# Performance work log

Measured on AMD Instinct MI355X. Metric: run time of the kernel, lower is better.

The kernel has to match this reference:

```python
import jax, jax.numpy as jnp
import numpy as np
import math

B, T, C = 2, 1024, 1024
H = 16
HS = C // H          # head size 64
ROT = HS // 2        # rotary dims 32
TT = 1024            # ctx_len
FFN = 4 * C
EPS = 1e-6


def _layernorm(x, g, b):
    m = jnp.mean(x, -1, keepdims=True)
    v = jnp.mean((x - m) ** 2, -1, keepdims=True)
    return (x - m) * jax.lax.rsqrt(v + EPS) * g + b


def _time_shift_half(x):
    # ZeroPad2d((0,0,1,-1)) applied to first half of channels: shift by one step in time
    c = x.shape[-1]
    a = jnp.pad(x[:, :, : c // 2], ((0, 0), (1, 0), (0, 0)))[:, :-1, :]
    return jnp.concatenate([a, x[:, :, c // 2 :]], axis=-1)


def _rotate_half(x):
    x1, x2 = jnp.split(x, 2, axis=-1)
    return jnp.concatenate([-x2, x1], axis=-1)


def _rotary_cos_sin(t_len, rot, base):
    inv_freq = 1.0 / (base ** (jnp.arange(0, rot, 2, dtype=jnp.float32) / rot))
    freqs = jnp.arange(t_len, dtype=jnp.float32)[:, None] * inv_freq[None, :]
    emb = jnp.concatenate([freqs, freqs], axis=-1)  # (T, rot)
    return jnp.cos(emb), jnp.sin(emb)


def _build_w(time_w, time_alpha, time_beta, t_len):
    # faithful translation of the pad/tile/reshape circulant trick
    w = jnp.pad(time_w, ((0, 0), (0, TT)))            # (H, 2TT)
    w = jnp.tile(w, (1, TT))                          # (H, 2TT*TT)
    w = w[:, :-TT].reshape(-1, TT, 2 * TT - 1)        # (H, TT, 2TT-1)
    w = w[:, :, TT - 1 :]                             # (H, TT, TT)
    return w[:, :t_len, :t_len] * time_alpha[:, :, :t_len] * time_beta[:, :t_len, :]


def setup_inputs() -> dict:
    key = jax.random.key(0)
    ks = jax.random.split(key, 24)
    s = 0.02
    d = {
        "x": jax.random.normal(ks[0], (B, T, C), jnp.float32),
        "ln1_g": jnp.ones((C,), jnp.float32),
        "ln1_b": jnp.zeros((C,), jnp.float32),
        "Wq": jax.random.normal(ks[1], (C, C), jnp.float32) * s,
        "bq": jnp.zeros((C,), jnp.float32),
        "Wk": jax.random.normal(ks[2], (C, C), jnp.float32) * s,
        "bk": jnp.zeros((C,), jnp.float32),
        "Wv": jax.random.normal(ks[3], (C, C), jnp.float32) * s,
        "bv": jnp.zeros((C,), jnp.float32),
        "Wo": jax.random.normal(ks[4], (C, C), jnp.float32) * s,
        "bo": jnp.zeros((C,), jnp.float32),
        "time_w": 1.0 + 0.01 * jax.random.normal(ks[5], (H, TT), jnp.float32),
        "time_alpha": 1.0 + 0.01 * jax.random.normal(ks[6], (H, 1, TT), jnp.float32),
        "time_beta": 1.0 + 0.01 * jax.random.normal(ks[7], (H, TT, 1), jnp.float32),
        "time_gamma": 1.0 + 0.01 * jax.random.normal(ks[8], (TT, 1), jnp.float32),
        "Wmix": jnp.eye(H, dtype=jnp.float32) + 0.01 * jax.random.normal(ks[9], (H, H), jnp.float32),
        "ln2_g": jnp.ones((C,), jnp.float32),
        "ln2_b": jnp.zeros((C,), jnp.float32),
        "Wgk": jax.random.normal(ks[10], (C, FFN), jnp.float32) * s,
        "bgk": jnp.zeros((FFN,), jnp.float32),
        "Wgv": jax.random.normal(ks[11], (C, FFN), jnp.float32) * s,
        "bgv": jnp.zeros((FFN,), jnp.float32),
        "Wgw": jax.random.normal(ks[12], (FFN, C), jnp.float32) * s,
        "bgw": jnp.zeros((C,), jnp.float32),
    }
    return d


def _block(x, ln1_g, ln1_b, Wq, bq, Wk, bk, Wv, bv, Wo, bo,
           time_w, time_alpha, time_beta, time_gamma, Wmix,
           ln2_g, ln2_b, Wgk, bgk, Wgv, bgv, Wgw, bgw):
    b, t, c = x.shape
    # ---- MHA_pro attention sublayer (pre-LN residual) ----
    xs = _time_shift_half(_layernorm(x, ln1_g, ln1_b))
    q = (xs @ Wq + bq).reshape(b, t, H, HS).transpose(0, 2, 1, 3)  # bhtd
    k = (xs @ Wk + bk).reshape(b, t, H, HS).transpose(0, 2, 1, 3)
    v = (xs @ Wv + bv).reshape(b, t, H, HS).transpose(0, 2, 1, 3)
    qr, qp = q[..., :ROT], q[..., ROT:]
    kr, kp = k[..., :ROT], k[..., ROT:]
    cos, sin = _rotary_cos_sin(t, ROT, float(TT))  # base = ctx_len
    qr = qr * cos + _rotate_half(qr) * sin
    kr = kr * cos + _rotate_half(kr) * sin
    q = jnp.concatenate([qr, qp], axis=-1)
    k = jnp.concatenate([kr, kp], axis=-1)
    att = jnp.einsum("bhtd,bhud->bhtu", q, k) * (1.0 / math.sqrt(HS))
    causal = jnp.tril(jnp.ones((t, t), bool))
    att = jnp.where(causal, att, -jnp.inf)
    att = jax.nn.softmax(att, axis=-1)
    w = _build_w(time_w, time_alpha, time_beta, t)  # (H, T, T)
    att = att * w[None]
    att = jnp.einsum("ij,bjtu->bitu", Wmix, att)  # 1x1 conv head mix
    y = jnp.einsum("bhtu,bhud->bhtd", att, v)
    y = y.transpose(0, 2, 1, 3).reshape(b, t, c)
    y = (y @ Wo + bo) * time_gamma[:t, :]
    x = x + y
    # ---- GeGLU MLP sublayer (pre-LN residual) ----
    xm = _layernorm(x, ln2_g, ln2_b)
    kk = xm @ Wgk + bgk
    vv = xm @ Wgv + bgv
    y2 = (jax.nn.gelu(kk, approximate=False) * vv) @ Wgw + bgw
    return x + y2


def reference(x, ln1_g, ln1_b, Wq, bq, Wk, bk, Wv, bv, Wo, bo,
              time_w, time_alpha, time_beta, time_gamma, Wmix,
              ln2_g, ln2_b, Wgk, bgk, Wgv, bgv, Wgw, bgw):
    return _block(x, ln1_g, ln1_b, Wq, bq, Wk, bk, Wv, bv, Wo, bo,
                  time_w, time_alpha, time_beta, time_gamma, Wmix,
                  ln2_g, ln2_b, Wgk, bgk, Wgv, bgv, Wgw, bgw)
```

## Files before the change

kernel.cpp:

```cpp
#include <hip/hip_runtime.h>
#include <math.h>

typedef unsigned short u16;
typedef short s16x8 __attribute__((ext_vector_type(8)));
typedef float f32x4 __attribute__((ext_vector_type(4)));

#define TB 2
#define TSEQ 1024
#define CC 1024
#define NH 16
#define HSZ 64
#define FFN 4096
#define MROWS (TB*TSEQ)

#define GLOAD16(g, l) __builtin_amdgcn_global_load_lds( \
    (const __attribute__((address_space(1))) unsigned*)(g), \
    (__attribute__((address_space(3))) unsigned*)(l), 16, 0, 0)

#define SBAR()  __builtin_amdgcn_s_barrier()
#define SCHED0() __builtin_amdgcn_sched_barrier(0)
#define LGKM0() asm volatile("s_waitcnt lgkmcnt(0)" ::: "memory")
#define WAITV4() asm volatile("s_waitcnt vmcnt(4)" ::: "memory")
#define PRIO(n) __builtin_amdgcn_s_setprio(n)

__device__ __forceinline__ float bf2f(u16 u){
  union { unsigned u; float f; } c; c.u = ((unsigned)u) << 16; return c.f;
}
__device__ __forceinline__ u16 f2bf(float f){
  union { float f; unsigned u; } c; c.f = f;
  unsigned u = c.u;
  u += 0x7fffu + ((u >> 16) & 1);
  return (u16)(u >> 16);
}
__device__ __forceinline__ float ldin(const void* p, size_t i, int bf){
  return bf ? bf2f(((const u16*)p)[i]) : ((const float*)p)[i];
}

__global__ void k_flag(const unsigned* __restrict__ g, int* __restrict__ flag){
  if (threadIdx.x == 0) *flag = (g[0] == 0x3F800000u) ? 0 : 1;
}

struct Prep {
  const void* csrc[10]; u16* cdst[10]; int cp0[11];
  const void* tw; u16* tw8; float2* rt;
};
__global__ void k_prep(Prep P, const int* __restrict__ flagp){
  int bf = *flagp;
  int blk = blockIdx.x, tid = threadIdx.x;
  if (blk < 184){
    int idx = blk*256 + tid;
    int s = 0;
    #pragma unroll
    for (int i = 1; i < 10; i++) if (idx >= P.cp0[i]) s = i;
    int r = idx - P.cp0[s];
    P.cdst[s][r] = f2bf(ldin(P.csrc[s], r, bf));
  } else if (blk < 696){
    int idx = (blk-184)*256 + tid;
    int s = idx >> 14;
    int h = (idx >> 10) & 15;
    int k = idx & 1023;
    float v = (k + s < 1024) ? ldin(P.tw, h*1024 + k + s, bf) : 0.f;
    P.tw8[idx] = f2bf(v);
  } else {
    int idx = (blk-696)*256 + tid;
    int i = idx & 15, t = idx >> 4;
    float invf = exp2f(-0.625f * (float)i);
    float ang = (float)t * invf;
    P.rt[idx] = (float2){cosf(ang), sinf(ang)};
  }
}

struct TEnt { const void* src; u16* dst; int R, C, bxn, blk0; };
struct TPack { TEnt e[7]; };
__global__ void k_transpose_all(TPack p, const int* __restrict__ flagp){
  int bf = *flagp;
  __shared__ u16 tile[32][33];
  int blk = blockIdx.x;
  int ei = 0;
  #pragma unroll
  for (int i = 1; i < 7; i++) if (blk >= p.e[i].blk0) ei = i;
  const void* src = p.e[ei].src;
  u16* dst = p.e[ei].dst;
  int R = p.e[ei].R, C = p.e[ei].C;
  int rel = blk - p.e[ei].blk0;
  int bx = (rel % p.e[ei].bxn) * 32, by = (rel / p.e[ei].bxn) * 32;
  int tx = threadIdx.x & 31, ty = threadIdx.x >> 5;
  #pragma unroll
  for (int i = 0; i < 32; i += 8)
    tile[ty + i][tx] = f2bf(ldin(src, (size_t)(by + ty + i) * C + bx + tx, bf));
  __syncthreads();
  #pragma unroll
  for (int i = 0; i < 32; i += 8)
    dst[(size_t)(bx + ty + i) * R + by + tx] = tile[tx][ty + i];
}

__global__ void k_ln1_shift(const void* __restrict__ x, const void* __restrict__ g,
                            const void* __restrict__ bta, u16* __restrict__ xs,
                            const int* __restrict__ flagp){
  int bf = *flagp;
  int row = blockIdx.x;
  int t = row & (TSEQ - 1);
  int tid = threadIdx.x;
  int wv = tid >> 6, lane = tid & 63;
  float v[4]; float s = 0.f, ss = 0.f;
  #pragma unroll
  for (int i = 0; i < 4; i++){
    v[i] = ldin(x, (size_t)row * CC + tid*4 + i, bf);
    s += v[i]; ss += v[i]*v[i];
  }
  #pragma unroll
  for (int o = 32; o > 0; o >>= 1){ s += __shfl_xor(s, o); ss += __shfl_xor(ss, o); }
  __shared__ float rs[4], rss[4];
  if (lane == 0){ rs[wv] = s; rss[wv] = ss; }
  __syncthreads();
  float S = rs[0]+rs[1]+rs[2]+rs[3];
  float SS = rss[0]+rss[1]+rss[2]+rss[3];
  float mean = S * (1.0f/CC);
  float var  = SS * (1.0f/CC) - mean*mean;
  float inv  = rsqrtf(var + 1e-6f);
  #pragma unroll
  for (int i = 0; i < 4; i++){
    int c = tid*4 + i;
    float o = (v[i]-mean)*inv*ldin(g, c, bf) + ldin(bta, c, bf);
    u16 ob = f2bf(o);
    if (c >= CC/2)            xs[(size_t)row*CC + c] = ob;
    else if (t < TSEQ-1)      xs[(size_t)(row+1)*CC + c] = ob;
  }
  if (t == 0 && tid < 128){
    #pragma unroll
    for (int i = 0; i < 4; i++) xs[(size_t)row*CC + tid*4 + i] = 0;
  }
}

__global__ __launch_bounds__(256) void k_qk(
    const u16* __restrict__ qkv, u16* __restrict__ att)
{
  int m0 = blockIdx.y * 128;
  int n0 = blockIdx.x * 128;
  if (n0 > m0) return;
  int bh = blockIdx.z; int b = bh >> 4, h = bh & 15;
  __shared__ u16 As[128*32];
  __shared__ u16 Bs[128*32];
  int tid = threadIdx.x;
  int w = tid >> 6;
  int lane = tid & 63;
  int wm = (w >> 1) * 64, wn = (w & 1) * 64;
  f32x4 acc[4][4];
  #pragma unroll
  for (int i = 0; i < 4; i++)
    #pragma unroll
    for (int j = 0; j < 4; j++) acc[i][j] = (f32x4){0.f,0.f,0.f,0.f};

  int rr = lane >> 2;
  int cc = lane & 3;
  const u16* gA0 = qkv + (size_t)(b*TSEQ + m0 + w*32 + rr)*(3*CC) + h*HSZ + cc*8;
  const u16* gA1 = gA0 + (size_t)16*(3*CC);
  const u16* gB0 = qkv + (size_t)(b*TSEQ + n0 + w*32 + rr)*(3*CC) + CC + h*HSZ + cc*8;
  const u16* gB1 = gB0 + (size_t)16*(3*CC);
  u16* lA0 = As + (w*32)*32;
  u16* lA1 = As + (w*32+16)*32;
  u16* lB0 = Bs + (w*32)*32;
  u16* lB1 = Bs + (w*32+16)*32;
  int quad = lane >> 4;
  int l15 = lane & 15;

  #pragma unroll
  for (int k0 = 0; k0 < HSZ; k0 += 32){
    __syncthreads();
    GLOAD16(gA0 + k0, lA0);
    GLOAD16(gA1 + k0, lA1);
    GLOAD16(gB0 + k0, lB0);
    GLOAD16(gB1 + k0, lB1);
    __syncthreads();
    s16x8 af[4], bfr[4];
    #pragma unroll
    for (int i = 0; i < 4; i++){
      af[i]  = *(s16x8*)&As[(wm + i*16 + l15)*32 + quad*8];
      bfr[i] = *(s16x8*)&Bs[(wn + i*16 + l15)*32 + quad*8];
    }
    #pragma unroll
    for (int mi = 0; mi < 4; mi++)
      #pragma unroll
      for (int ni = 0; ni < 4; ni++)
        acc[mi][ni] = __builtin_amdgcn_mfma_f32_16x16x32_bf16(af[mi], bfr[ni], acc[mi][ni], 0, 0, 0);
  }

  #pragma unroll
  for (int mi = 0; mi < 4; mi++){
    int rowb = m0 + wm + mi*16 + quad*4;
    #pragma unroll
    for (int ni = 0; ni < 4; ni++){
      int col = n0 + wn + ni*16 + l15;
      #pragma unroll
      for (int r = 0; r < 4; r++){
        int t = rowb + r;
        att[((size_t)bh*TSEQ + t)*TSEQ + col] = f2bf(acc[mi][ni][r] * 0.125f);
      }
    }
  }
}

__global__ __launch_bounds__(1024) void k_softmix(
    u16* __restrict__ att, const u16* __restrict__ tw8, const u16* __restrict__ al16,
    const u16* __restrict__ be16, const void* __restrict__ wmix,
    const int* __restrict__ flagp)
{
  int bf = *flagp;
  int bt = blockIdx.x;
  int t = bt & (TSEQ-1);
  int b = bt >> 10;
  int tid = threadIdx.x;
  int h = tid >> 6;
  int lane = tid & 63;
  int tile_end = ((t >> 7) + 1) << 7;
  int nchunk = (t >> 9) + 1;
  int sh = (TSEQ-1 - t) & 7;
  int base = (TSEQ-1 - t) - sh;
  __shared__ __align__(16) u16 P[NH][TSEQ];
  __shared__ float wm[NH*NH];
  if (tid < NH*NH) wm[tid] = ldin(wmix, tid, bf);

  {
    const u16* srow = att + ((size_t)(b*NH + h)*TSEQ + t)*TSEQ;
    const u16* twp  = tw8 + ((size_t)sh*NH + h)*TSEQ + base;
    const u16* alp  = al16 + h*TSEQ;
    float v[16];
    float lmax = -1e30f;
    for (int r = 0; r < nchunk; r++){
      int ub = lane*8 + r*512;
      uint4 pk = *(const uint4*)(srow + ub);
      const u16* pe = (const u16*)&pk;
      #pragma unroll
      for (int e = 0; e < 8; e++){
        float s = bf2f(pe[e]);
        if (ub + e > t) s = -1e30f;
        v[r*8+e] = s;
        lmax = fmaxf(lmax, s);
      }
    }
    #pragma unroll
    for (int o = 32; o > 0; o >>= 1) lmax = fmaxf(lmax, __shfl_xor(lmax, o));
    float lsum = 0.f;
    for (int r = 0; r < nchunk; r++){
      #pragma unroll
      for (int e = 0; e < 8; e++){
        float p = __expf(v[r*8+e] - lmax);
        v[r*8+e] = p; lsum += p;
      }
    }
    #pragma unroll
    for (int o = 32; o > 0; o >>= 1) lsum += __shfl_xor(lsum, o);
    float btv = bf2f(be16[h*TSEQ + t]);
    float inv = btv / lsum;
    for (int r = 0; r < nchunk; r++){
      int ub = lane*8 + r*512;
      uint4 wk = *(const uint4*)(twp + ub);
      uint4 ak = *(const uint4*)(alp + ub);
      const u16* we = (const u16*)&wk;
      const u16* ae = (const u16*)&ak;
      u16 tmp[8];
      #pragma unroll
      for (int e = 0; e < 8; e++){
        float p = v[r*8+e] * inv * bf2f(we[e]) * bf2f(ae[e]);
        tmp[e] = f2bf(p);
      }
      *(uint4*)&P[h][ub] = *(uint4*)tmp;
    }
  }
  __syncthreads();

  int u0 = tid * 2;
  if (u0 < tile_end){
    float a0_[16], a1_[16];
    #pragma unroll
    for (int i = 0; i < 16; i++){ a0_[i] = 0.f; a1_[i] = 0.f; }
    #pragma unroll
    for (int j = 0; j < 16; j++){
      unsigned pk = *(const unsigned*)&P[j][u0];
      float p0 = bf2f((u16)(pk & 0xffff)), p1 = bf2f((u16)(pk >> 16));
      #pragma unroll
      for (int i = 0; i < 16; i++){
        float w = wm[i*NH + j];
        a0_[i] += w*p0; a1_[i] += w*p1;
      }
    }
    #pragma unroll
    for (int i = 0; i < 16; i++){
      u16 tmp[2] = {f2bf(a0_[i]), f2bf(a1_[i])};
      *(unsigned*)(att + ((size_t)(b*NH + i)*TSEQ + t)*TSEQ + u0) = *(unsigned*)tmp;
    }
  }
}

__global__ void k_vt(const u16* __restrict__ qkv, u16* __restrict__ vt){
  __shared__ u16 tile[32][33];
  int bh = blockIdx.z; int b = bh >> 4, h = bh & 15;
  int u0 = blockIdx.x * 32, d0 = blockIdx.y * 32;
  int tx = threadIdx.x & 31, ty = threadIdx.x >> 5;
  #pragma unroll
  for (int i = 0; i < 32; i += 8)
    tile[ty + i][tx] = qkv[(size_t)(b*TSEQ + u0 + ty + i)*(3*CC) + 2*CC + h*HSZ + d0 + tx];
  __syncthreads();
  #pragma unroll
  for (int i = 0; i < 32; i += 8)
    vt[((size_t)bh*HSZ + d0 + ty + i)*TSEQ + u0 + tx] = tile[tx][ty + i];
}

__global__ void k_gelumul(const u16* __restrict__ kkvv, u16* __restrict__ hh){
  int idx = blockIdx.x*256 + threadIdx.x;
  int m = idx >> 9;
  int j = (idx & 511) * 8;
  uint4 kk4 = *(const uint4*)(kkvv + (size_t)m*(2*FFN) + j);
  uint4 vv4 = *(const uint4*)(kkvv + (size_t)m*(2*FFN) + FFN + j);
  const u16* ks = (const u16*)&kk4;
  const u16* vs = (const u16*)&vv4;
  u16 out[8];
  #pragma unroll
  for (int e = 0; e < 8; e++){
    float kk = bf2f(ks[e]), vv = bf2f(vs[e]);
    float ge = 0.5f*kk*(1.0f + erff(kk*0.70710678f));
    out[e] = f2bf(ge*vv);
  }
  *(uint4*)(hh + (size_t)m*FFN + j) = *(uint4*)out;
}

__global__ __launch_bounds__(512, 2) void k_gemm256(
    const u16* __restrict__ A, const u16* __restrict__ Bt,
    const u16* __restrict__ bias, int M, int N, int K, int mode,
    u16* __restrict__ outp, float* __restrict__ partial,
    const float2* __restrict__ rt)
{
  __shared__ u16 S[65536];
  u16* SA0 = S;
  u16* SB0 = S + 16384;
  u16* SA1 = S + 32768;
  u16* SB1 = S + 49152;

  int nwg = (int)(gridDim.x * gridDim.y * gridDim.z);
  int lin = (int)(blockIdx.x + gridDim.x * (blockIdx.y + gridDim.y * blockIdx.z));
  int nl  = (nwg & 7) ? lin : ((lin & 7) * (nwg >> 3) + (lin >> 3));
  int bx  = nl % (int)gridDim.x;
  int tq  = nl / (int)gridDim.x;
  int by  = tq % (int)gridDim.y;
  int bz  = tq / (int)gridDim.y;

  int m0 = by * 256, n0 = bx * 256;
  int kper = K / (int)gridDim.z;
  int kbeg = bz * kper;
  int nt = kper >> 6;
  int niter = nt >> 1;

  int tid = threadIdx.x;
  int w = tid >> 6, lane = tid & 63;
  int wm = w >> 2, wn = w & 3;
  int quad = lane >> 4, l15 = lane & 15;
  int l3 = lane >> 3, ch = (lane & 7) ^ l3;

  const u16* gA = A  + (size_t)(m0 + w*16 + l3) * K + ch*8 + kbeg;
  const u16* gB = Bt + (size_t)(n0 + w*16 + l3) * K + ch*8 + kbeg;
  const size_t hstep = (size_t)128 * K;
  const size_t rstep = (size_t)8 * K;

  int pc0 = quad ^ (l15 & 7);
  int pc1 = (4 + quad) ^ (l15 & 7);
  int aoff0 = (wm*128 + l15)*64 + pc0*8;
  int aoff1 = (wm*128 + l15)*64 + pc1*8;
  int boff0 = (wn*64 + l15)*64 + pc0*8;
  int boff1 = (wn*64 + l15)*64 + pc1*8;

  f32x4 acc[8][4];
  #pragma unroll
  for (int i = 0; i < 8; i++)
    #pragma unroll
    for (int j = 0; j < 4; j++) acc[i][j] = (f32x4){0.f,0.f,0.f,0.f};

  #define STG(gbase, sbase, h, ko) do{ \
      const u16* _g = (gbase) + (size_t)(h)*hstep + (ko); \
      u16* _l = (sbase) + ((h)*128 + w*16)*64; \
      GLOAD16(_g, _l); \
      GLOAD16(_g + rstep, _l + 512); \
    }while(0)

  #define LD_A(buf, MQ) do{ _Pragma("unroll") for (int _m = 0; _m < 4; _m++){ \
      a0[_m] = *(const s16x8*)((buf) + aoff0 + (MQ)*4096 + _m*1024); \
      a1[_m] = *(const s16x8*)((buf) + aoff1 + (MQ)*4096 + _m*1024); } }while(0)

  #define LD_B(buf, NQ, B0A, B1A) do{ _Pragma("unroll") for (int _n = 0; _n < 2; _n++){ \
      B0A[_n] = *(const s16x8*)((buf) + boff0 + (NQ)*2048 + _n*1024); \
      B1A[_n] = *(const s16x8*)((buf) + boff1 + (NQ)*2048 + _n*1024); } }while(0)

  #define MMQ(MQ, NQ, B0A, B1A) do{ _Pragma("unroll") for (int _m = 0; _m < 4; _m++){ \
      _Pragma("unroll") for (int _n = 0; _n < 2; _n++){ \
        acc[(MQ)*4+_m][(NQ)*2+_n] = __builtin_amdgcn_mfma_f32_16x16x32_bf16(a0[_m], B0A[_n], acc[(MQ)*4+_m][(NQ)*2+_n], 0, 0, 0); \
        acc[(MQ)*4+_m][(NQ)*2+_n] = __builtin_amdgcn_mfma_f32_16x16x32_bf16(a1[_m], B1A[_n], acc[(MQ)*4+_m][(NQ)*2+_n], 0, 0, 0); }} }while(0)

  STG(gB, SB0, 0, 0); STG(gB, SB0, 1, 0);
  STG(gA, SA0, 0, 0); STG(gA, SA0, 1, 0);
  STG(gB, SB1, 0, 64); STG(gB, SB1, 1, 64);
  WAITV4();
  SBAR();

  s16x8 a0[4], a1[4], bl0[2], bl1[2], bh0[2], bh1[2];

  for (int i = 0; i < niter; i++){
    int t1k = (2*i+1)*64;
    int t2k = (2*i+2 < nt) ? (2*i+2)*64 : 0;
    int t3k = (2*i+3 < nt) ? (2*i+3)*64 : 0;

    LD_A(SA0, 0); LD_B(SB0, 0, bl0, bl1);
    STG(gA, SA1, 0, t1k);
    SBAR(); LGKM0(); SCHED0(); PRIO(1); MMQ(0,0,bl0,bl1); PRIO(0); SBAR();
    LD_B(SB0, 1, bh0, bh1);
    STG(gA, SA1, 1, t1k);
    SBAR(); LGKM0(); SCHED0(); PRIO(1); MMQ(0,1,bh0,bh1); PRIO(0); SBAR();
    LD_A(SA0, 1);
    STG(gB, SB0, 0, t2k);
    SBAR(); LGKM0(); SCHED0(); PRIO(1); MMQ(1,0,bl0,bl1); PRIO(0); SBAR();
    STG(gB, SB0, 1, t2k);
    SBAR(); LGKM0(); SCHED0(); PRIO(1); MMQ(1,1,bh0,bh1); PRIO(0);
    WAITV4(); SBAR();
    LD_A(SA1, 0); LD_B(SB1, 0, bl0, bl1);
    STG(gA, SA0, 0, t2k);
    SBAR(); LGKM0(); SCHED0(); PRIO(1); MMQ(0,0,bl0,bl1); PRIO(0); SBAR();
    LD_B(SB1, 1, bh0, bh1);
    STG(gA, SA0, 1, t2k);
    SBAR(); LGKM0(); SCHED0(); PRIO(1); MMQ(0,1,bh0,bh1); PRIO(0); SBAR();
    LD_A(SA1, 1);
    STG(gB, SB1, 0, t3k);
    SBAR(); LGKM0(); SCHED0(); PRIO(1); MMQ(1,0,bl0,bl1); PRIO(0); SBAR();
    STG(gB, SB1, 1, t3k);
    SBAR(); LGKM0(); SCHED0(); PRIO(1); MMQ(1,1,bh0,bh1); PRIO(0);
    WAITV4(); SBAR();
  }

  if (mode == 3){
    float* pout = partial + (size_t)bz * M * N;
    #pragma unroll
    for (int mi = 0; mi < 8; mi++){
      int rowb = m0 + wm*128 + mi*16 + quad*4;
      #pragma unroll
      for (int ni = 0; ni < 4; ni++){
        int col = n0 + wn*64 + ni*16 + l15;
        #pragma unroll
        for (int r = 0; r < 4; r++)
          pout[(size_t)(rowb + r) * N + col] = acc[mi][ni][r];
      }
    }
  } else if (mode == 5){
    int col0 = n0 + wn*64;
    int rot = (col0 < 2048);
    float bv0 = bf2f(bias[col0 + l15]);
    float bv1 = bf2f(bias[col0 + 16 + l15]);
    float bv2 = bf2f(bias[col0 + 32 + l15]);
    float bv3 = bf2f(bias[col0 + 48 + l15]);
    #pragma unroll
    for (int mi = 0; mi < 8; mi++){
      int rowb = m0 + wm*128 + mi*16 + quad*4;
      #pragma unroll
      for (int r = 0; r < 4; r++){
        int row = rowb + r;
        int t = row & (TSEQ-1);
        float v0 = acc[mi][0][r] + bv0;
        float v1 = acc[mi][1][r] + bv1;
        if (rot){
          float2 cs = rt[t*16 + l15];
          float o0 = v0*cs.x - v1*cs.y;
          v1 = v1*cs.x + v0*cs.y;
          v0 = o0;
        }
        size_t rbase = (size_t)row * N + col0;
        outp[rbase + l15]      = f2bf(v0);
        outp[rbase + 16 + l15] = f2bf(v1);
        outp[rbase + 32 + l15] = f2bf(acc[mi][2][r] + bv2);
        outp[rbase + 48 + l15] = f2bf(acc[mi][3][r] + bv3);
      }
    }
  } else {
    #pragma unroll
    for (int mi = 0; mi < 8; mi++){
      int rowb = m0 + wm*128 + mi*16 + quad*4;
      #pragma unroll
      for (int ni = 0; ni < 4; ni++){
        int col = n0 + wn*64 + ni*16 + l15;
        float bv = bf2f(bias[col]);
        #pragma unroll
        for (int r = 0; r < 4; r++)
          outp[(size_t)(rowb + r) * N + col] = f2bf(acc[mi][ni][r] + bv);
      }
    }
  }
  #undef STG
  #undef LD_A
  #undef LD_B
  #undef MMQ
}

__global__ void k_reduceK(const float* __restrict__ partial, int nsplit,
                          int M, int N, const u16* __restrict__ bias, int mode,
                          void* __restrict__ outp, const void* __restrict__ xres,
                          const float* __restrict__ resf, const u16* __restrict__ gamma,
                          const void* __restrict__ g2, const void* __restrict__ b2,
                          u16* __restrict__ xm, const int* __restrict__ flagp){
  int bf = *flagp;
  int idx = blockIdx.x*256 + threadIdx.x;
  int row = idx / (N/4);
  int c0  = (idx % (N/4)) * 4;
  size_t base = (size_t)row * N + c0;
  float v[4] = {0.f, 0.f, 0.f, 0.f};
  for (int s = 0; s < nsplit; s++){
    const float4 p = *(const float4*)(partial + (size_t)s * M * N + base);
    v[0] += p.x; v[1] += p.y; v[2] += p.z; v[3] += p.w;
  }
  #pragma unroll
  for (int e = 0; e < 4; e++) v[e] += bf2f(bias[c0 + e]);
  if (mode == 1){
    int t = row & (TSEQ-1);
    float gm = bf2f(gamma[t]);
    float o[4];
    #pragma unroll
    for (int e = 0; e < 4; e++) o[e] = ldin(xres, base + e, bf) + v[e] * gm;
    *(float4*)((float*)outp + base) = (float4){o[0], o[1], o[2], o[3]};
    int tid = threadIdx.x;
    int wv = tid >> 6, lane = tid & 63;
    float s = o[0]+o[1]+o[2]+o[3];
    float ss = o[0]*o[0]+o[1]*o[1]+o[2]*o[2]+o[3]*o[3];
    #pragma unroll
    for (int off = 32; off > 0; off >>= 1){ s += __shfl_xor(s, off); ss += __shfl_xor(ss, off); }
    __shared__ float rs[4], rss[4];
    if (lane == 0){ rs[wv] = s; rss[wv] = ss; }
    __syncthreads();
    float S = rs[0]+rs[1]+rs[2]+rs[3];
    float SS = rss[0]+rss[1]+rss[2]+rss[3];
    float mean = S * (1.0f/CC);
    float var  = SS * (1.0f/CC) - mean*mean;
    float inv  = rsqrtf(var + 1e-6f);
    u16 tmp[4];
    #pragma unroll
    for (int e = 0; e < 4; e++){
      int c = c0 + e;
      tmp[e] = f2bf((o[e]-mean)*inv*ldin(g2, c, bf) + ldin(b2, c, bf));
    }
    *(uint2*)(xm + base) = *(uint2*)tmp;
  } else {
    float o[4];
    #pragma unroll
    for (int e = 0; e < 4; e++) o[e] = resf[base + e] + v[e];
    if (bf){
      u16 tmp[4] = {f2bf(o[0]), f2bf(o[1]), f2bf(o[2]), f2bf(o[3])};
      *(uint2*)((u16*)outp + base) = *(uint2*)tmp;
    } else {
      *(float4*)((float*)outp + base) = (float4){o[0], o[1], o[2], o[3]};
    }
  }
}

__global__ __launch_bounds__(256) void k_pv(
    const u16* __restrict__ att, const u16* __restrict__ vt, u16* __restrict__ y)
{
  __shared__ u16 As[128*32];
  __shared__ u16 Bs[64*32];
  int tid = threadIdx.x;
  int bh = blockIdx.y; int b = bh >> 4, h = bh & 15;
  int m0 = blockIdx.x * 128;
  const u16* A  = att + (size_t)bh * TSEQ * TSEQ;
  const u16* Bt = vt  + (size_t)bh * HSZ * TSEQ;
  int w = tid >> 6;
  int lane = tid & 63;
  int wm = (w >> 1) * 64, wn = (w & 1) * 32;
  f32x4 acc[4][2];
  #pragma unroll
  for (int i = 0; i < 4; i++){ acc[i][0] = (f32x4){0,0,0,0}; acc[i][1] = (f32x4){0,0,0,0}; }

  int rr = lane >> 2;
  int cc = lane & 3;
  const u16* gA0 = A + (size_t)(m0 + w*32 + rr)*TSEQ + cc*8;
  const u16* gA1 = gA0 + (size_t)16*TSEQ;
  const u16* gB0 = Bt + (size_t)(w*16 + rr)*TSEQ + cc*8;
  u16* lA0 = As + (w*32)*32;
  u16* lA1 = As + (w*32+16)*32;
  u16* lB0 = Bs + (w*16)*32;
  int quad = lane >> 4;
  int l15 = lane & 15;
  int kend = m0 + 128;

  for (int k0 = 0; k0 < kend; k0 += 32){
    __syncthreads();
    GLOAD16(gA0 + k0, lA0);
    GLOAD16(gA1 + k0, lA1);
    GLOAD16(gB0 + k0, lB0);
    __syncthreads();
    s16x8 af[4], bfr[2];
    #pragma unroll
    for (int i = 0; i < 4; i++)
      af[i] = *(s16x8*)&As[(wm + i*16 + l15)*32 + quad*8];
    #pragma unroll
    for (int i = 0; i < 2; i++)
      bfr[i] = *(s16x8*)&Bs[(wn + i*16 + l15)*32 + quad*8];
    #pragma unroll
    for (int mi = 0; mi < 4; mi++)
      #pragma unroll
      for (int ni = 0; ni < 2; ni++)
        acc[mi][ni] = __builtin_amdgcn_mfma_f32_16x16x32_bf16(af[mi], bfr[ni], acc[mi][ni], 0, 0, 0);
  }

  #pragma unroll
  for (int mi = 0; mi < 4; mi++){
    int rowb = m0 + wm + mi*16 + quad*4;
    #pragma unroll
    for (int ni = 0; ni < 2; ni++){
      int col = wn + ni*16 + l15;
      #pragma unroll
      for (int r = 0; r < 4; r++){
        int t = rowb + r;
        y[(size_t)(b*TSEQ + t)*CC + h*HSZ + col] = f2bf(acc[mi][ni][r]);
      }
    }
  }
}

extern "C" void kernel_launch(void* const* d_in, const int* in_sizes, int n_in,
                              void* d_out, int out_size, void* d_ws, size_t ws_size,
                              hipStream_t stream){
  const void* x     = d_in[0];
  const void* ln1g  = d_in[1];
  const void* ln1b  = d_in[2];
  const void* Wq    = d_in[3];
  const void* bq    = d_in[4];
  const void* Wk    = d_in[5];
  const void* bk    = d_in[6];
  const void* Wv    = d_in[7];
  const void* bv    = d_in[8];
  const void* Wo    = d_in[9];
  const void* bo    = d_in[10];
  const void* timew = d_in[11];
  const void* alpha = d_in[12];
  const void* beta  = d_in[13];
  const void* gamma = d_in[14];
  const void* Wmix  = d_in[15];
  const void* ln2g  = d_in[16];
  const void* ln2b  = d_in[17];
  const void* Wgk   = d_in[18];
  const void* bgk   = d_in[19];
  const void* Wgv   = d_in[20];
  const void* bgv   = d_in[21];
  const void* Wgw   = d_in[22];
  const void* bgw   = d_in[23];

  char* ws = (char*)d_ws;
  size_t off = 0;
  auto carve = [&](size_t bytes)->char*{
    char* p = ws + off; off = (off + bytes + 255) & ~(size_t)255; return p;
  };
  int*  FLAG   = (int*)carve(256);
  u16*  WT_QKV = (u16*)carve(3072ull*1024*2);
  u16*  WT_O   = (u16*)carve(1024ull*1024*2);
  u16*  WT_G   = (u16*)carve(8192ull*1024*2);
  u16*  WT_W   = (u16*)carve(1024ull*4096*2);
  u16*  B_QKV  = (u16*)carve(3072*2);
  u16*  B_G    = (u16*)carve(8192*2);
  u16*  B_O    = (u16*)carve(1024*2);
  u16*  B_W    = (u16*)carve(1024*2);
  u16*  GMA    = (u16*)carve(1024*2);
  u16*  TW8    = (u16*)carve(8ull*16*1024*2 + 4096);
  u16*  AL16   = (u16*)carve(16*1024*2);
  u16*  BE16   = (u16*)carve(16*1024*2);
  u16*  XS     = (u16*)carve((size_t)MROWS*CC*2);
  u16*  QKV    = (u16*)carve((size_t)MROWS*3*CC*2);
  u16*  ATT    = (u16*)carve((size_t)TB*NH*TSEQ*TSEQ*2);
  u16*  VT     = (u16*)carve((size_t)TB*NH*HSZ*TSEQ*2);
  u16*  Y      = (u16*)carve((size_t)MROWS*CC*2);
  float* X1    = (float*)carve((size_t)MROWS*CC*4);
  u16*  XM     = (u16*)carve((size_t)MROWS*CC*2);
  u16*  KKVV   = (u16*)carve((size_t)MROWS*2*FFN*2);
  u16*  HH     = (u16*)carve((size_t)MROWS*FFN*2);
  float2* RT   = (float2*)carve((size_t)TSEQ*16*8);
  float* PART  = (float*)ATT;
  (void)ws_size; (void)in_sizes; (void)n_in; (void)out_size;

  k_flag<<<1,64,0,stream>>>((const unsigned*)ln1g, FLAG);

  Prep P;
  P.csrc[0]=bq;    P.cdst[0]=B_QKV;
  P.csrc[1]=bk;    P.cdst[1]=B_QKV+1024;
  P.csrc[2]=bv;    P.cdst[2]=B_QKV+2048;
  P.csrc[3]=bgk;   P.cdst[3]=B_G;
  P.csrc[4]=bgv;   P.cdst[4]=B_G+4096;
  P.csrc[5]=bo;    P.cdst[5]=B_O;
  P.csrc[6]=bgw;   P.cdst[6]=B_W;
  P.csrc[7]=gamma; P.cdst[7]=GMA;
  P.csrc[8]=alpha; P.cdst[8]=AL16;
  P.csrc[9]=beta;  P.cdst[9]=BE16;
  int sizes[10] = {1024,1024,1024,4096,4096,1024,1024,1024,16384,16384};
  int acc0 = 0;
  for (int i = 0; i < 10; i++){ P.cp0[i] = acc0; acc0 += sizes[i]; }
  P.cp0[10] = acc0;
  P.tw = timew; P.tw8 = TW8; P.rt = RT;
  k_prep<<<760,256,0,stream>>>(P, FLAG);

  TPack T;
  T.e[0] = {Wq,  WT_QKV,                1024, 1024,  32,     0};
  T.e[1] = {Wk,  WT_QKV + 1024*1024,    1024, 1024,  32,  1024};
  T.e[2] = {Wv,  WT_QKV + 2*1024*1024,  1024, 1024,  32,  2048};
  T.e[3] = {Wo,  WT_O,                  1024, 1024,  32,  3072};
  T.e[4] = {Wgk, WT_G,                  1024, 4096, 128,  4096};
  T.e[5] = {Wgv, WT_G + 4096ull*1024,   1024, 4096, 128,  8192};
  T.e[6] = {Wgw, WT_W,                  4096, 1024,  32, 12288};
  k_transpose_all<<<16384,256,0,stream>>>(T, FLAG);

  k_ln1_shift<<<MROWS,256,0,stream>>>(x, ln1g, ln1b, XS, FLAG);
  k_gemm256<<<dim3(12,8),512,0,stream>>>(XS, WT_QKV, B_QKV, MROWS, 3072, 1024, 5,
                                         QKV, nullptr, RT);
  k_qk<<<dim3(8,8,TB*NH),256,0,stream>>>(QKV, ATT);
  k_softmix<<<TB*TSEQ,1024,0,stream>>>(ATT, TW8, AL16, BE16, Wmix, FLAG);
  k_vt<<<dim3(32,2,32),256,0,stream>>>(QKV, VT);
  k_pv<<<dim3(8,32),256,0,stream>>>(ATT, VT, Y);

  k_gemm256<<<dim3(4,8,4),512,0,stream>>>(Y, WT_O, nullptr, MROWS, 1024, 1024, 3,
                                          nullptr, PART, nullptr);
  k_reduceK<<<MROWS*1024/(4*256),256,0,stream>>>(PART, 4, MROWS, 1024, B_O, 1,
                                                 X1, x, nullptr, GMA,
                                                 ln2g, ln2b, XM, FLAG);

  k_gemm256<<<dim3(32,8),512,0,stream>>>(XM, WT_G, B_G, MROWS, 8192, 1024, 0,
                                         KKVV, nullptr, nullptr);
  k_gelumul<<<(MROWS*FFN)/(256*8),256,0,stream>>>(KKVV, HH);

  k_gemm256<<<dim3(4,8,8),512,0,stream>>>(HH, WT_W, nullptr, MROWS, 1024, 4096, 3,
                                          nullptr, PART, nullptr);
  k_reduceK<<<MROWS*1024/(4*256),256,0,stream>>>(PART, 8, MROWS, 1024, B_W, 2,
                                                 d_out, nullptr, X1, nullptr,
                                                 nullptr, nullptr, nullptr, FLAG);
}
```

Measured before the change: 402.3 us.

## Fuse GeGLU gelu-multiply into gate GEMM epilogue via interleaved weight layout

Interleaves the Wgk and Wgv transposed weight rows and their biases in 16-column groups, so each GEMM wave's accumulator tiles hold matching k and v columns. A new epilogue mode applies bias, exact-erf GELU and the multiply in registers and writes the half-width hidden activation directly. This removes the separate gelu-multiply kernel and the write and re-read of the 2x-wide KKVV intermediate. The cost is erff evaluation inside the GEMM epilogue and scattered 2-byte stores.

```diff
diff --git a/kernel.cpp b/kernel.cpp
--- a/kernel.cpp
+++ b/kernel.cpp
@@ -53,7 +53,10 @@
     #pragma unroll
     for (int i = 1; i < 10; i++) if (idx >= P.cp0[i]) s = i;
     int r = idx - P.cp0[s];
-    P.cdst[s][r] = f2bf(ldin(P.csrc[s], r, bf));
+    int d = r;
+    if (s == 3)      d = ((r>>4)<<5) | (r&15);
+    else if (s == 4) d = ((r>>4)<<5) | 16 | (r&15);
+    P.cdst[s][d] = f2bf(ldin(P.csrc[s], r, bf));
   } else if (blk < 696){
     int idx = (blk-184)*256 + tid;
     int s = idx >> 14;
@@ -70,7 +73,7 @@
   }
 }
 
-struct TEnt { const void* src; u16* dst; int R, C, bxn, blk0; };
+struct TEnt { const void* src; u16* dst; int R, C, bxn, blk0, perm; };
 struct TPack { TEnt e[7]; };
 __global__ void k_transpose_all(TPack p, const int* __restrict__ flagp){
   int bf = *flagp;
@@ -81,7 +84,7 @@
   for (int i = 1; i < 7; i++) if (blk >= p.e[i].blk0) ei = i;
   const void* src = p.e[ei].src;
   u16* dst = p.e[ei].dst;
-  int R = p.e[ei].R, C = p.e[ei].C;
+  int R = p.e[ei].R, C = p.e[ei].C, perm = p.e[ei].perm;
   int rel = blk - p.e[ei].blk0;
   int bx = (rel % p.e[ei].bxn) * 32, by = (rel / p.e[ei].bxn) * 32;
   int tx = threadIdx.x & 31, ty = threadIdx.x >> 5;
@@ -90,8 +93,13 @@
     tile[ty + i][tx] = f2bf(ldin(src, (size_t)(by + ty + i) * C + bx + tx, bf));
   __syncthreads();
   #pragma unroll
-  for (int i = 0; i < 32; i += 8)
-    dst[(size_t)(bx + ty + i) * R + by + tx] = tile[tx][ty + i];
+  for (int i = 0; i < 32; i += 8){
+    int c = bx + ty + i;
+    int rowo = c;
+    if (perm == 1)      rowo = ((c>>4)<<5) | (c&15);
+    else if (perm == 2) rowo = ((c>>4)<<5) | 16 | (c&15);
+    dst[(size_t)rowo * R + by + tx] = tile[tx][ty + i];
+  }
 }
 
 __global__ void k_ln1_shift(const void* __restrict__ x, const void* __restrict__ g,
@@ -304,24 +312,6 @@
   #pragma unroll
   for (int i = 0; i < 32; i += 8)
     vt[((size_t)bh*HSZ + d0 + ty + i)*TSEQ + u0 + tx] = tile[tx][ty + i];
-}
-
-__global__ void k_gelumul(const u16* __restrict__ kkvv, u16* __restrict__ hh){
-  int idx = blockIdx.x*256 + threadIdx.x;
-  int m = idx >> 9;
-  int j = (idx & 511) * 8;
-  uint4 kk4 = *(const uint4*)(kkvv + (size_t)m*(2*FFN) + j);
-  uint4 vv4 = *(const uint4*)(kkvv + (size_t)m*(2*FFN) + FFN + j);
-  const u16* ks = (const u16*)&kk4;
-  const u16* vs = (const u16*)&vv4;
-  u16 out[8];
-  #pragma unroll
-  for (int e = 0; e < 8; e++){
-    float kk = bf2f(ks[e]), vv = bf2f(vs[e]);
-    float ge = 0.5f*kk*(1.0f + erff(kk*0.70710678f));
-    out[e] = f2bf(ge*vv);
-  }
-  *(uint4*)(hh + (size_t)m*FFN + j) = *(uint4*)out;
 }
 
 __global__ __launch_bounds__(512, 2) void k_gemm256(
@@ -444,6 +434,26 @@
         #pragma unroll
         for (int r = 0; r < 4; r++)
           pout[(size_t)(rowb + r) * N + col] = acc[mi][ni][r];
+      }
+    }
+  } else if (mode == 4){
+    int Nout = N >> 1;
+    #pragma unroll
+    for (int mi = 0; mi < 8; mi++){
+      int rowb = m0 + wm*128 + mi*16 + quad*4;
+      #pragma unroll
+      for (int nip = 0; nip < 2; nip++){
+        int ckk = n0 + wn*64 + (2*nip)*16 + l15;
+        int jcol = (n0 >> 1) + wn*32 + nip*16 + l15;
+        float bk = bf2f(bias[ckk]);
+        float bvv = bf2f(bias[ckk + 16]);
+        #pragma unroll
+        for (int r = 0; r < 4; r++){
+          float kk = acc[mi][2*nip][r] + bk;
+          float vv = acc[mi][2*nip+1][r] + bvv;
+          float ge = 0.5f*kk*(1.0f + erff(kk*0.70710678f));
+          outp[(size_t)(rowb + r) * Nout + jcol] = f2bf(ge*vv);
+        }
       }
     }
   } else if (mode == 5){
@@ -671,7 +681,6 @@
   u16*  Y      = (u16*)carve((size_t)MROWS*CC*2);
   float* X1    = (float*)carve((size_t)MROWS*CC*4);
   u16*  XM     = (u16*)carve((size_t)MROWS*CC*2);
-  u16*  KKVV   = (u16*)carve((size_t)MROWS*2*FFN*2);
   u16*  HH     = (u16*)carve((size_t)MROWS*FFN*2);
   float2* RT   = (float2*)carve((size_t)TSEQ*16*8);
   float* PART  = (float*)ATT;
@@ -684,7 +693,7 @@
   P.csrc[1]=bk;    P.cdst[1]=B_QKV+1024;
   P.csrc[2]=bv;    P.cdst[2]=B_QKV+2048;
   P.csrc[3]=bgk;   P.cdst[3]=B_G;
-  P.csrc[4]=bgv;   P.cdst[4]=B_G+4096;
+  P.csrc[4]=bgv;   P.cdst[4]=B_G;
   P.csrc[5]=bo;    P.cdst[5]=B_O;
   P.csrc[6]=bgw;   P.cdst[6]=B_W;
   P.csrc[7]=gamma; P.cdst[7]=GMA;
@@ -698,13 +707,13 @@
   k_prep<<<760,256,0,stream>>>(P, FLAG);
 
   TPack T;
-  T.e[0] = {Wq,  WT_QKV,                1024, 1024,  32,     0};
-  T.e[1] = {Wk,  WT_QKV + 1024*1024,    1024, 1024,  32,  1024};
-  T.e[2] = {Wv,  WT_QKV + 2*1024*1024,  1024, 1024,  32,  2048};
-  T.e[3] = {Wo,  WT_O,                  1024, 1024,  32,  3072};
-  T.e[4] = {Wgk, WT_G,                  1024, 4096, 128,  4096};
-  T.e[5] = {Wgv, WT_G + 4096ull*1024,   1024, 4096, 128,  8192};
-  T.e[6] = {Wgw, WT_W,                  4096, 1024,  32, 12288};
+  T.e[0] = {Wq,  WT_QKV,                1024, 1024,  32,     0, 0};
+  T.e[1] = {Wk,  WT_QKV + 1024*1024,    1024, 1024,  32,  1024, 0};
+  T.e[2] = {Wv,  WT_QKV + 2*1024*1024,  1024, 1024,  32,  2048, 0};
+  T.e[3] = {Wo,  WT_O,                  1024, 1024,  32,  3072, 0};
+  T.e[4] = {Wgk, WT_G,                  1024, 4096, 128,  4096, 1};
+  T.e[5] = {Wgv, WT_G,                  1024, 4096, 128,  8192, 2};
+  T.e[6] = {Wgw, WT_W,                  4096, 1024,  32, 12288, 0};
   k_transpose_all<<<16384,256,0,stream>>>(T, FLAG);
 
   k_ln1_shift<<<MROWS,256,0,stream>>>(x, ln1g, ln1b, XS, FLAG);
@@ -721,9 +730,8 @@
                                                  X1, x, nullptr, GMA,
                                                  ln2g, ln2b, XM, FLAG);
 
-  k_gemm256<<<dim3(32,8),512,0,stream>>>(XM, WT_G, B_G, MROWS, 8192, 1024, 0,
-                                         KKVV, nullptr, nullptr);
-  k_gelumul<<<(MROWS*FFN)/(256*8),256,0,stream>>>(KKVV, HH);
+  k_gemm256<<<dim3(32,8),512,0,stream>>>(XM, WT_G, B_G, MROWS, 8192, 1024, 4,
+                                         HH, nullptr, nullptr);
 
   k_gemm256<<<dim3(4,8,8),512,0,stream>>>(HH, WT_W, nullptr, MROWS, 1024, 4096, 3,
                                           nullptr, PART, nullptr);
```

Result: no change. 401.7 us (-0.2%).
